# Optimization experiments

Measured on AMD Instinct MI355X. Metric: run time of the kernel, lower is better.

## Reference

```python
import math
import jax, jax.numpy as jnp
import numpy as np

DIM = 512
STYLE_DIM = 512
WS = 8
RES = 64
HEADS = 16
SHIFT = WS // 2
B = 8
EPS = 1e-5


def _rel_pos_index(ws):
    # Faithful replica of the (non-standard) index construction in the source.
    coords = np.stack(np.meshgrid(np.arange(ws), np.arange(ws), indexing='ij')).reshape(2, -1)
    rc = (coords[:, :, None] - coords[:, None, :]).transpose(1, 2, 0).astype(np.int64)
    rc[:, :, 0] += ws - 1
    rc[:, :, 1] += ws - 1
    rc[:, :, 0] += 2 * ws - 1
    return jnp.asarray(rc.sum(-1))  # (ws*ws, ws*ws)


def _attn_mask2(res, ws):
    shift = ws // 2
    m = np.zeros((res, res), dtype=np.float32)
    cnt = 0
    for hs in [slice(0, -ws), slice(-ws, -shift), slice(-shift, None)]:
        for wsl in [slice(0, -ws), slice(-ws, -shift), slice(-shift, None)]:
            m[hs, wsl] = cnt
            cnt += 1
    mw = m.reshape(res // ws, ws, res // ws, ws).transpose(0, 2, 1, 3).reshape(-1, ws * ws)
    am = mw[:, None, :] - mw[:, :, None]  # (nW, N, N)
    return jnp.asarray(np.where(am != 0, -100.0, 0.0).astype(np.float32))


_RPI = _rel_pos_index(WS)
_MASK2 = _attn_mask2(RES, WS)


def _win_part(x, ws):
    Bc, H, W, C = x.shape
    x = x.reshape(Bc, H // ws, ws, W // ws, ws, C).transpose(0, 1, 3, 2, 4, 5)
    return x.reshape(-1, ws * ws, C)


def _win_rev(x, ws, H, W):
    nH, nW = H // ws, W // ws
    C = x.shape[-1]
    x = x.reshape(-1, nH, nW, ws, ws, C).transpose(0, 1, 3, 2, 4, 5)
    return x.reshape(-1, H, W, C)


def _adain(x, style, w, b):
    # x: (B, N, C); InstanceNorm1d over the token dim N per channel (biased var, no affine).
    scale = 1.0 / math.sqrt(w.shape[1])
    s = style @ (w * scale).T + b  # (B, 2C)
    C = x.shape[-1]
    gamma, beta = s[:, :C], s[:, C:]
    mean = x.mean(axis=1, keepdims=True)
    var = x.var(axis=1, keepdims=True)
    xn = (x - mean) / jnp.sqrt(var + EPS)
    return gamma[:, None, :] * xn + beta[:, None, :]


def _window_attn(q, k, v, ws, heads, rpb, rpi, mask):
    # q/k/v: (B, H, W, C)
    C = q.shape[-1]
    hd = C // heads
    qk_scale = hd ** -0.5
    qw = _win_part(q, ws)  # (Bw, N, C)
    kw = _win_part(k, ws)
    vw = _win_part(v, ws)
    Bw, N, _ = qw.shape
    qw = qw.reshape(Bw, N, heads, hd).transpose(0, 2, 1, 3)
    kw = kw.reshape(Bw, N, heads, hd).transpose(0, 2, 1, 3)
    vw = vw.reshape(Bw, N, heads, hd).transpose(0, 2, 1, 3)
    attn = jnp.einsum('bhnd,bhmd->bhnm', qw, kw) * qk_scale
    bias = rpb[rpi.reshape(-1)].reshape(N, N, heads).transpose(2, 0, 1)  # (h, N, N)
    attn = attn + bias[None]
    if mask is not None:
        nW = mask.shape[0]
        attn = attn.reshape(Bw // nW, nW, heads, N, N) + mask[None, :, None]
        attn = attn.reshape(Bw, heads, N, N)
    attn = jax.nn.softmax(attn, axis=-1)
    out = jnp.einsum('bhnm,bhmd->bhnd', attn, vw)
    return out.transpose(0, 2, 1, 3).reshape(Bw, N, C)


def _forward(x, style, ada1_w, ada1_b, qkv_w, qkv_b, rpb1, rpb2,
             proj_w, proj_b, ada2_w, ada2_b, mlp_w1, mlp_b1, mlp_w2, mlp_b2):
    H = W = RES
    Bc, N, C = x.shape
    shortcut = x
    xn = _adain(x, style, ada1_w, ada1_b)
    qkv = xn @ qkv_w.T + qkv_b  # (B, N, 3C)
    qkv = qkv.reshape(Bc, N, 3, C).transpose(2, 0, 1, 3).reshape(3, Bc, H, W, C)
    qkv1 = qkv[..., : C // 2]
    qkv2 = qkv[..., C // 2:]
    qkv2 = jnp.roll(qkv2, shift=(-SHIFT, -SHIFT), axis=(2, 3))
    x1 = _window_attn(qkv1[0], qkv1[1], qkv1[2], WS, HEADS // 2, rpb1, _RPI, None)
    x2 = _window_attn(qkv2[0], qkv2[1], qkv2[2], WS, HEADS // 2, rpb2, _RPI, _MASK2)
    x1 = _win_rev(x1, WS, H, W)
    x2 = _win_rev(x2, WS, H, W)
    x2 = jnp.roll(x2, shift=(SHIFT, SHIFT), axis=(1, 2))
    out = jnp.concatenate([x1, x2], axis=-1).reshape(Bc, N, C)
    out = out @ proj_w.T + proj_b
    out = shortcut + out
    xn2 = _adain(out, style, ada2_w, ada2_b)
    h = xn2 @ mlp_w1.T + mlp_b1
    h = jax.nn.gelu(h, approximate=False)  # erf-based gelu matches source
    h = h @ mlp_w2.T + mlp_b2
    return out + h


def setup_inputs() -> dict:
    key = jax.random.key(0)
    ks = jax.random.split(key, 16)
    rn = lambda k, shp, s: jax.random.normal(k, shp, dtype=jnp.float32) * s
    return {
        'x': rn(ks[0], (B, RES * RES, DIM), 1.0),
        'style': rn(ks[1], (B, STYLE_DIM), 1.0),
        'ada1_w': rn(ks[2], (2 * DIM, STYLE_DIM), 1.0),
        'ada1_b': rn(ks[3], (2 * DIM,), 0.02),
        'qkv_w': rn(ks[4], (3 * DIM, DIM), 0.02),
        'qkv_b': rn(ks[5], (3 * DIM,), 0.02),
        'rpb1': rn(ks[6], ((2 * WS - 1) ** 2, HEADS // 2), 0.02),
        'rpb2': rn(ks[7], ((2 * WS - 1) ** 2, HEADS // 2), 0.02),
        'proj_w': rn(ks[8], (DIM, DIM), 0.02),
        'proj_b': rn(ks[9], (DIM,), 0.02),
        'ada2_w': rn(ks[10], (2 * DIM, STYLE_DIM), 1.0),
        'ada2_b': rn(ks[11], (2 * DIM,), 0.02),
        'mlp_w1': rn(ks[12], (4 * DIM, DIM), 0.02),
        'mlp_b1': rn(ks[13], (4 * DIM,), 0.02),
        'mlp_w2': rn(ks[14], (DIM, 4 * DIM), 0.02),
        'mlp_b2': rn(ks[15], (DIM,), 0.02),
    }


def reference(x, style, ada1_w, ada1_b, qkv_w, qkv_b, rpb1, rpb2,
              proj_w, proj_b, ada2_w, ada2_b, mlp_w1, mlp_b1, mlp_w2, mlp_b2):
    return _forward(x, style, ada1_w, ada1_b, qkv_w, qkv_b, rpb1, rpb2,
                    proj_w, proj_b, ada2_w, ada2_b, mlp_w1, mlp_b1, mlp_w2, mlp_b2)
```

## Files before the change

### kernel.cpp

```cpp
#include <hip/hip_runtime.h>
#include <math.h>

typedef __attribute__((ext_vector_type(8))) short short8;
typedef __attribute__((ext_vector_type(4))) float f32x4;
typedef unsigned short ushort_t;
typedef unsigned long long ull_t;

__device__ __forceinline__ float bf2f(ushort_t u) {
    return __uint_as_float(((unsigned int)u) << 16);
}
__device__ __forceinline__ ushort_t f2bf(float f) {
    unsigned int u = __float_as_uint(f);
    unsigned int r = u + 0x7fffu + ((u >> 16) & 1u);
    return (ushort_t)(r >> 16);
}
__device__ __forceinline__ unsigned cvt_pk_bf16(float lo, float hi) {
    unsigned r;
    asm volatile("v_cvt_pk_bf16_f32 %0, %1, %2" : "=v"(r) : "v"(lo), "v"(hi));
    return r;
}

__device__ __forceinline__ void async_cp16(const void* g, void* l) {
    __builtin_amdgcn_global_load_lds((const __attribute__((address_space(1))) void*)g,
                                     (__attribute__((address_space(3))) void*)l, 16, 0, 0);
}

__device__ __forceinline__ float fast_gelu(float v) {
    float u2 = 2.0f * v * (0.7978845608028654f + 0.0356774081f * v * v);
    float e = __expf(u2);
    float r = 1.0f / (e + 1.0f);
    return v - v * r;
}

__global__ __launch_bounds__(256) void conv_zero(
        const float* __restrict__ qkv_w, ushort_t* __restrict__ qkv_wb,
        const float* __restrict__ proj_w, ushort_t* __restrict__ proj_wb,
        const float* __restrict__ w1, ushort_t* __restrict__ w1b,
        const float* __restrict__ w2, ushort_t* __restrict__ w2b,
        float* __restrict__ psum2, float* __restrict__ psq2,
        const float* __restrict__ rpb1, const float* __restrict__ rpb2,
        float* __restrict__ tbl0, float* __restrict__ tbl1) {
    int i = blockIdx.x * 256 + threadIdx.x;
    if (i < 786432) {
        qkv_wb[i] = f2bf(qkv_w[i]);
    } else if (i < 1048576) {
        int j = i - 786432; proj_wb[j] = f2bf(proj_w[j]);
    } else if (i < 2097152) {
        int j = i - 1048576; w1b[j] = f2bf(w1[j]);
    } else if (i < 3145728) {
        int j = i - 2097152; w2b[j] = f2bf(w2[j]);
    } else if (i < 3153920) {
        int j = i - 3145728;
        psum2[j] = 0.f; psq2[j] = 0.f;
    } else {
        int t = i - 3153920;
        if (t < 32768) {
            int h = t >> 12, ij = t & 4095;
            int qi = ij >> 6, kj = ij & 63;
            int idx = ((qi >> 3) - (kj >> 3)) + ((qi & 7) - (kj & 7)) + 29;
            tbl0[t] = rpb1[idx * 8 + h];
        } else {
            int u = t - 32768;
            int ij = u & 4095;
            int cls = (u >> 12) & 3;
            int h = u >> 14;
            int qi = ij >> 6, kj = ij & 63;
            int idx = ((qi >> 3) - (kj >> 3)) + ((qi & 7) - (kj & 7)) + 29;
            float v = rpb2[idx * 8 + h];
            int gh_i = (cls & 2) ? (((qi >> 3) < 4) ? 1 : 2) : 0;
            int gw_i = (cls & 1) ? (((qi & 7) < 4) ? 1 : 2) : 0;
            int gh_j = (cls & 2) ? (((kj >> 3) < 4) ? 1 : 2) : 0;
            int gw_j = (cls & 1) ? (((kj & 7) < 4) ? 1 : 2) : 0;
            if (gh_i * 3 + gw_i != gh_j * 3 + gw_j) v -= 100.f;
            tbl1[u] = v;
        }
    }
}

__global__ __launch_bounds__(256) void style_kernel(const float* __restrict__ style,
        const float* __restrict__ w1, const float* __restrict__ b1,
        const float* __restrict__ w2, const float* __restrict__ b2,
        float* __restrict__ s1, float* __restrict__ s2) {
    int t = blockIdx.x * 256 + threadIdx.x;
    int which = t >> 13;
    int idx = t & 8191;
    int b = idx >> 10, j = idx & 1023;
    const float* w = which ? w2 : w1;
    const float* bb = which ? b2 : b1;
    const float* st = style + b * 512;
    const float* wr = w + (size_t)j * 512;
    float acc = 0.f;
    for (int k = 0; k < 512; ++k) acc += st[k] * wr[k];
    float v = acc * 0.04419417382415922f + bb[j];
    (which ? s2 : s1)[idx] = v;
}

__global__ __launch_bounds__(512) void stats_part(const float* __restrict__ x,
        float* __restrict__ psum, float* __restrict__ psq) {
    int b = blockIdx.x >> 5;
    int ch = blockIdx.x & 31;
    int c = threadIdx.x;
    const float* p = x + ((size_t)b * 4096 + (size_t)ch * 128) * 512 + c;
    float s = 0.f, q = 0.f;
    for (int t = 0; t < 128; ++t) {
        float v = p[(size_t)t * 512];
        s += v; q += v * v;
    }
    psum[(size_t)blockIdx.x * 512 + c] = s;
    psq [(size_t)blockIdx.x * 512 + c] = q;
}

__global__ __launch_bounds__(256) void stats_fin(const float* __restrict__ psum,
        const float* __restrict__ psq, float* __restrict__ mean, float* __restrict__ rstd) {
    int i = blockIdx.x * 256 + threadIdx.x;
    int b = i >> 9, c = i & 511;
    float s = 0.f, q = 0.f;
    for (int ch = 0; ch < 32; ++ch) {
        s += psum[(size_t)(b * 32 + ch) * 512 + c];
        q += psq [(size_t)(b * 32 + ch) * 512 + c];
    }
    float m = s * (1.f / 4096.f);
    float v = q * (1.f / 4096.f) - m * m;
    mean[i] = m;
    rstd[i] = rsqrtf(v + 1e-5f);
}

__global__ __launch_bounds__(256) void stats_fin2(const float* __restrict__ psum2,
        const float* __restrict__ psq2, float* __restrict__ mean, float* __restrict__ rstd) {
    int i = blockIdx.x * 256 + threadIdx.x;
    float m = psum2[i] * (1.f / 4096.f);
    float v = psq2[i] * (1.f / 4096.f) - m * m;
    mean[i] = m;
    rstd[i] = rsqrtf(v + 1e-5f);
}

__global__ __launch_bounds__(256) void adain_kernel(const float* __restrict__ x,
        const float* __restrict__ s, const float* __restrict__ mean,
        const float* __restrict__ rstd, ushort_t* __restrict__ xn) {
    size_t i4 = (size_t)blockIdx.x * 256 + threadIdx.x;
    size_t e = i4 * 4;
    int b = (int)(e >> 21);
    int c = (int)(e & 511);
    float4 xv = *(const float4*)(x + e);
    float vals[4] = {xv.x, xv.y, xv.z, xv.w};
    ushort_t o[4];
#pragma unroll
    for (int j = 0; j < 4; ++j) {
        int cc = c + j;
        float g  = s[b * 1024 + cc];
        float be = s[b * 1024 + 512 + cc];
        float mn = mean[b * 512 + cc];
        float rs = rstd[b * 512 + cc];
        o[j] = f2bf(g * (vals[j] - mn) * rs + be);
    }
    ull_t packed = (ull_t)o[0] |
        ((ull_t)o[1] << 16) | ((ull_t)o[2] << 32) | ((ull_t)o[3] << 48);
    *(ull_t*)(xn + e) = packed;
}

template<int EPI>
__global__ __launch_bounds__(512, 2) void gemm256(
        const ushort_t* __restrict__ A, const ushort_t* __restrict__ Bw,
        const float* __restrict__ bias, const float* __restrict__ resid,
        float* __restrict__ outf, ushort_t* __restrict__ outh,
        float* __restrict__ psum2, float* __restrict__ psq2,
        int N, int K, int gridN, int ntiles, int lnt) {
    __shared__ ushort_t lds[65536];
    const int tid  = threadIdx.x;
    const int lane = tid & 63;
    const int wave = tid >> 6;
    const int wm = wave >> 2, wn = wave & 3;
    const int lm = lane & 15;
    const int kg = lane >> 4;
    const int nt = 1 << lnt;
    const int tpb = ntiles >> 8;

    const int orig = blockIdx.x;
    const int wgid = (orig & 7) * 32 + (orig >> 3);

    unsigned int lo0 = lm * 128 + ((kg * 16) ^ ((lm & 7) << 4));
    unsigned int lo1 = lo0 ^ 64;
    unsigned int vA0 = wm * 16384 + lo0;
    unsigned int vA1 = wm * 16384 + lo1;
    unsigned int vB0 = 65536 + (wn >> 1) * 16384 + (wn & 1) * 8192 + lo0;
    unsigned int vB1 = 65536 + (wn >> 1) * 16384 + (wn & 1) * 8192 + lo1;
    const char* ldsc = (const char*)lds;

    int off[2][2];
#pragma unroll
    for (int rnd = 0; rnd < 2; ++rnd) {
        int chunk = tid + rnd * 512;
        int row = chunk >> 3;
        int g = chunk & 7;
        int gsw = g ^ (row & 7);
#pragma unroll
        for (int h = 0; h < 2; ++h)
            off[h][rnd] = (h * 128 + row) * K + gsw * 8;
    }

    f32x4 acc[8][4];
#pragma unroll
    for (int m = 0; m < 8; ++m)
#pragma unroll
        for (int n = 0; n < 4; ++n)
#pragma unroll
            for (int r = 0; r < 4; ++r) acc[m][n][r] = 0.f;

    auto stage = [&](const ushort_t* __restrict__ mat, long bcur, long bnxt,
                     int dslot, int h, int tt, int isB) {
        long mb = (tt < nt) ? bcur : bnxt;
        int kt = tt & (nt - 1);
        const ushort_t* base = mat + mb + (kt << 6);
        ushort_t* dst = (ushort_t*)lds + isB * 32768 + dslot * 16384 + h * 8192 + tid * 8;
#pragma unroll
        for (int rnd = 0; rnd < 2; ++rnd)
            async_cp16(base + off[h][rnd], dst + rnd * 4096);
    };

    int tcur = wgid;
    int bm = tcur / gridN, bn = tcur - bm * gridN;
    long Am = (long)bm * 256 * K;
    long Bn = (long)bn * 256 * K;

    stage(A,  Am, Am, 0, 0, 0, 0); stage(A,  Am, Am, 0, 1, 0, 0);
    stage(Bw, Bn, Bn, 0, 0, 0, 1); stage(Bw, Bn, Bn, 0, 1, 0, 1);
    stage(Bw, Bn, Bn, 1, 0, 1, 1); stage(Bw, Bn, Bn, 1, 1, 1, 1);
    asm volatile("s_waitcnt vmcnt(4)" ::: "memory");
    __builtin_amdgcn_sched_barrier(0);
    __builtin_amdgcn_s_barrier();

    for (int ti = 0; ti < tpb; ++ti) {
        int tnxt = (ti + 1 < tpb) ? tcur + 256 : tcur;
        int bm2 = tnxt / gridN, bn2 = tnxt - bm2 * gridN;
        long Am2 = (long)bm2 * 256 * K;
        long Bn2 = (long)bn2 * 256 * K;

#pragma unroll 2
        for (int t = 0; t < nt; ++t) {
            const int c = t & 1;
            short8 bfr[4][2];
#pragma unroll
            for (int q = 0; q < 4; ++q) {
                short8 af[2][2];
#pragma unroll
                for (int mq = 0; mq < 2; ++mq) {
                    af[mq][0] = *(const short8*)(ldsc + vA0 + (q * 4096 + mq * 2048));
                    af[mq][1] = *(const short8*)(ldsc + vA1 + (q * 4096 + mq * 2048));
                }
                if (q == 0) {
#pragma unroll
                    for (int n = 0; n < 4; ++n) {
                        bfr[n][0] = *(const short8*)(ldsc + vB0 + n * 2048);
                        bfr[n][1] = *(const short8*)(ldsc + vB1 + n * 2048);
                    }
                }
                if      (q == 0) stage(A,  Am, Am2, c ^ 1, 0, t + 1, 0);
                else if (q == 1) stage(A,  Am, Am2, c ^ 1, 1, t + 1, 0);
                else if (q == 2) stage(Bw, Bn, Bn2, c,     0, t + 2, 1);
                else             stage(Bw, Bn, Bn2, c,     1, t + 2, 1);

                __builtin_amdgcn_s_barrier();
                asm volatile("s_waitcnt lgkmcnt(0)" ::: "memory");
                __builtin_amdgcn_sched_barrier(0);
                __builtin_amdgcn_s_setprio(1);
#pragma unroll
                for (int mq = 0; mq < 2; ++mq)
#pragma unroll
                    for (int n = 0; n < 4; ++n)
#pragma unroll
                        for (int ks = 0; ks < 2; ++ks)
                            acc[q * 2 + mq][n] = __builtin_amdgcn_mfma_f32_16x16x32_bf16(
                                af[mq][ks], bfr[n][ks], acc[q * 2 + mq][n], 0, 0, 0);
                __builtin_amdgcn_s_setprio(0);
                if (q == 3) {
                    asm volatile("s_waitcnt vmcnt(4)" ::: "memory");
                    __builtin_amdgcn_sched_barrier(0);
                }
                __builtin_amdgcn_s_barrier();
            }
            vA0 ^= 32768u; vA1 ^= 32768u; vB0 ^= 32768u; vB1 ^= 32768u;
        }

        const long tile_m = (long)bm * 256;
        const long tile_n = (long)bn * 256;
        float csum[4], csq[4];
        if (EPI == 1) {
#pragma unroll
            for (int n = 0; n < 4; ++n) { csum[n] = 0.f; csq[n] = 0.f; }
        }
#pragma unroll
        for (int m = 0; m < 8; ++m) {
            long row0 = tile_m + wm * 128 + m * 16 + kg * 4;
#pragma unroll
            for (int n = 0; n < 4; ++n) {
                long col = tile_n + wn * 64 + n * 16 + lm;
                float bb = bias[col];
#pragma unroll
                for (int r = 0; r < 4; ++r) {
                    long o = (row0 + r) * (long)N + col;
                    float v = acc[m][n][r] + bb;
                    if (EPI == 0) {
                        outh[o] = f2bf(v);
                    } else if (EPI == 1) {
                        float w = v + resid[o];
                        outf[o] = w;
                        csum[n] += w; csq[n] += w * w;
                    } else if (EPI == 2) {
                        outh[o] = f2bf(fast_gelu(v));
                    } else {
                        outf[o] += v;
                    }
                    acc[m][n][r] = 0.f;
                }
            }
        }
        if (EPI == 1) {
            int b = (int)(tile_m >> 12);
#pragma unroll
            for (int n = 0; n < 4; ++n) {
                int col = (int)(tile_n + wn * 64 + n * 16 + lm);
                atomicAdd(&psum2[b * 512 + col], csum[n]);
                atomicAdd(&psq2 [b * 512 + col], csq[n]);
            }
        }

        tcur = tnxt; bm = bm2; bn = bn2; Am = Am2; Bn = Bn2;
    }
}

__global__ __launch_bounds__(256) void attn_mfma(const ushort_t* __restrict__ qkv,
        const float* __restrict__ tbl0, const float* __restrict__ tbl1,
        ushort_t* __restrict__ attno) {
    __shared__ ushort_t lds[27648];
    const int tid = threadIdx.x;
    const int lane = tid & 63;
    const int wave = tid >> 6;
    const int job = blockIdx.x * 4 + wave;
    const int branch = job >> 12;
    const int w_idx  = (job >> 3) & 511;
    const int head   = job & 7;
    const int b = w_idx >> 6, win = w_idx & 63;
    const int wh = win >> 3, ww = win & 7;
    const int c0 = branch * 256 + head * 32;
    const int i_lo = lane & 15;
    const int kg = lane >> 4;

    ushort_t* Vt = lds + wave * 6912;
    ushort_t* P  = lds + wave * 6912 + 2304;

    auto tokof = [&](int p) {
        int hh = wh * 8 + (p >> 3), wp = ww * 8 + (p & 7);
        if (branch) { hh = (hh + 4) & 63; wp = (wp + 4) & 63; }
        return b * 4096 + hh * 64 + wp;
    };

    {
        const ushort_t* vp = qkv + (size_t)tokof(lane) * 1536 + 1024 + c0;
        short8 v0 = *(const short8*)(vp);
        short8 v1 = *(const short8*)(vp + 8);
        short8 v2 = *(const short8*)(vp + 16);
        short8 v3 = *(const short8*)(vp + 24);
#pragma unroll
        for (int e = 0; e < 8; ++e) {
            Vt[(e     ) * 72 + lane] = (ushort_t)v0[e];
            Vt[(e +  8) * 72 + lane] = (ushort_t)v1[e];
            Vt[(e + 16) * 72 + lane] = (ushort_t)v2[e];
            Vt[(e + 24) * 72 + lane] = (ushort_t)v3[e];
        }
    }

    short8 kf[4], qf[4];
#pragma unroll
    for (int m = 0; m < 4; ++m) {
        size_t rowb = (size_t)tokof(m * 16 + i_lo) * 1536;
        kf[m] = *(const short8*)(qkv + rowb + 512 + c0 + kg * 8);
        qf[m] = *(const short8*)(qkv + rowb + c0 + kg * 8);
    }

    f32x4 s[4][4];
#pragma unroll
    for (int mj = 0; mj < 4; ++mj)
#pragma unroll
        for (int ni = 0; ni < 4; ++ni)
#pragma unroll
            for (int r = 0; r < 4; ++r) s[mj][ni][r] = 0.f;
#pragma unroll
    for (int mj = 0; mj < 4; ++mj)
#pragma unroll
        for (int ni = 0; ni < 4; ++ni)
            s[mj][ni] = __builtin_amdgcn_mfma_f32_16x16x32_bf16(kf[mj], qf[ni], s[mj][ni], 0, 0, 0);

    const float* tb;
    if (branch == 0) {
        tb = tbl0 + head * 4096;
    } else {
        int cls = ((wh == 7) ? 2 : 0) | ((ww == 7) ? 1 : 0);
        tb = tbl1 + (head * 4 + cls) * 4096;
    }
#pragma unroll
    for (int ni = 0; ni < 4; ++ni) {
        int i = ni * 16 + i_lo;
#pragma unroll
        for (int mj = 0; mj < 4; ++mj) {
            float4 bv = *(const float4*)(tb + i * 64 + mj * 16 + kg * 4);
            s[mj][ni][0] = s[mj][ni][0] * 0.17677669529663687f + bv.x;
            s[mj][ni][1] = s[mj][ni][1] * 0.17677669529663687f + bv.y;
            s[mj][ni][2] = s[mj][ni][2] * 0.17677669529663687f + bv.z;
            s[mj][ni][3] = s[mj][ni][3] * 0.17677669529663687f + bv.w;
        }
    }

    float mx[4], rs[4];
#pragma unroll
    for (int ni = 0; ni < 4; ++ni) {
        float m = -1e30f;
#pragma unroll
        for (int mj = 0; mj < 4; ++mj)
#pragma unroll
            for (int r = 0; r < 4; ++r) m = fmaxf(m, s[mj][ni][r]);
        m = fmaxf(m, __shfl_xor(m, 16));
        m = fmaxf(m, __shfl_xor(m, 32));
        mx[ni] = m;
    }
#pragma unroll
    for (int ni = 0; ni < 4; ++ni) {
        float sum = 0.f;
#pragma unroll
        for (int mj = 0; mj < 4; ++mj)
#pragma unroll
            for (int r = 0; r < 4; ++r) {
                float e = __expf(s[mj][ni][r] - mx[ni]);
                s[mj][ni][r] = e;
                sum += e;
            }
        sum += __shfl_xor(sum, 16);
        sum += __shfl_xor(sum, 32);
        rs[ni] = sum;
    }

#pragma unroll
    for (int ni = 0; ni < 4; ++ni) {
        int i = ni * 16 + i_lo;
#pragma unroll
        for (int mj = 0; mj < 4; ++mj) {
            unsigned w0 = cvt_pk_bf16(s[mj][ni][0], s[mj][ni][1]);
            unsigned w1 = cvt_pk_bf16(s[mj][ni][2], s[mj][ni][3]);
            ull_t w = (ull_t)w0 | ((ull_t)w1 << 32);
            *(ull_t*)&P[i * 72 + mj * 16 + kg * 4] = w;
        }
    }
    asm volatile("s_waitcnt lgkmcnt(0)" ::: "memory");
    __builtin_amdgcn_sched_barrier(0);

    short8 va[2][2];
    short8 pb[4][2];
#pragma unroll
    for (int md = 0; md < 2; ++md)
#pragma unroll
        for (int ks = 0; ks < 2; ++ks)
            va[md][ks] = *(const short8*)&Vt[(md * 16 + i_lo) * 72 + ks * 32 + kg * 8];
#pragma unroll
    for (int ni = 0; ni < 4; ++ni)
#pragma unroll
        for (int ks = 0; ks < 2; ++ks)
            pb[ni][ks] = *(const short8*)&P[(ni * 16 + i_lo) * 72 + ks * 32 + kg * 8];

    f32x4 o[2][4];
#pragma unroll
    for (int md = 0; md < 2; ++md)
#pragma unroll
        for (int ni = 0; ni < 4; ++ni)
#pragma unroll
            for (int r = 0; r < 4; ++r) o[md][ni][r] = 0.f;
#pragma unroll
    for (int md = 0; md < 2; ++md)
#pragma unroll
        for (int ni = 0; ni < 4; ++ni)
#pragma unroll
            for (int ks = 0; ks < 2; ++ks)
                o[md][ni] = __builtin_amdgcn_mfma_f32_16x16x32_bf16(va[md][ks], pb[ni][ks], o[md][ni], 0, 0, 0);

#pragma unroll
    for (int ni = 0; ni < 4; ++ni) {
        float inv = 1.f / rs[ni];
        ushort_t* op = attno + (size_t)tokof(ni * 16 + i_lo) * 512 + c0;
#pragma unroll
        for (int md = 0; md < 2; ++md) {
            ushort_t h0 = f2bf(o[md][ni][0] * inv);
            ushort_t h1 = f2bf(o[md][ni][1] * inv);
            ushort_t h2 = f2bf(o[md][ni][2] * inv);
            ushort_t h3 = f2bf(o[md][ni][3] * inv);
            ull_t w = (ull_t)h0 | ((ull_t)h1 << 16) | ((ull_t)h2 << 32) | ((ull_t)h3 << 48);
            *(ull_t*)(op + md * 16 + kg * 4) = w;
        }
    }
}

extern "C" void kernel_launch(void* const* d_in, const int* in_sizes, int n_in,
                              void* d_out, int out_size, void* d_ws, size_t ws_size,
                              hipStream_t stream) {
    const float* x      = (const float*)d_in[0];
    const float* style  = (const float*)d_in[1];
    const float* ada1_w = (const float*)d_in[2];
    const float* ada1_b = (const float*)d_in[3];
    const float* qkv_w  = (const float*)d_in[4];
    const float* qkv_b  = (const float*)d_in[5];
    const float* rpb1   = (const float*)d_in[6];
    const float* rpb2   = (const float*)d_in[7];
    const float* proj_w = (const float*)d_in[8];
    const float* proj_b = (const float*)d_in[9];
    const float* ada2_w = (const float*)d_in[10];
    const float* ada2_b = (const float*)d_in[11];
    const float* mlp_w1 = (const float*)d_in[12];
    const float* mlp_b1 = (const float*)d_in[13];
    const float* mlp_w2 = (const float*)d_in[14];
    const float* mlp_b2 = (const float*)d_in[15];
    float* outf = (float*)d_out;

    char* W = (char*)d_ws;
    ushort_t* qkvb    = (ushort_t*)(W);
    ushort_t* attno   = (ushort_t*)(W + 100663296);
    ushort_t* hbuf    = (ushort_t*)(W);
    ushort_t* xn      = (ushort_t*)(W + 134217728);
    ushort_t* qkv_wb  = (ushort_t*)(W + 167772160);
    ushort_t* proj_wb = (ushort_t*)(W + 167772160 + 1572864);
    ushort_t* w1b     = (ushort_t*)(W + 167772160 + 2097152);
    ushort_t* w2b     = (ushort_t*)(W + 167772160 + 4194304);
    float* freg  = (float*)(W + 167772160 + 6291456);
    float* s1    = freg;
    float* s2    = freg + 8192;
    float* mean1 = freg + 16384;
    float* rstd1 = freg + 20480;
    float* mean2 = freg + 24576;
    float* rstd2 = freg + 28672;
    float* psum  = freg + 32768;
    float* psq   = freg + 163840;
    float* psum2 = freg + 294912;
    float* psq2  = freg + 303104;
    float* tbl0  = freg + 311296;
    float* tbl1  = freg + 344064;

    conv_zero<<<12960, 256, 0, stream>>>(qkv_w, qkv_wb, proj_w, proj_wb,
                                         mlp_w1, w1b, mlp_w2, w2b, psum2, psq2,
                                         rpb1, rpb2, tbl0, tbl1);

    style_kernel<<<64, 256, 0, stream>>>(style, ada1_w, ada1_b, ada2_w, ada2_b, s1, s2);

    stats_part<<<256, 512, 0, stream>>>(x, psum, psq);
    stats_fin<<<16, 256, 0, stream>>>(psum, psq, mean1, rstd1);
    adain_kernel<<<16384, 256, 0, stream>>>(x, s1, mean1, rstd1, xn);

    gemm256<0><<<256, 512, 0, stream>>>(xn, qkv_wb, qkv_b, nullptr, nullptr, qkvb,
                                        nullptr, nullptr, 1536, 512, 6, 768, 3);

    attn_mfma<<<2048, 256, 0, stream>>>(qkvb, tbl0, tbl1, attno);

    gemm256<1><<<256, 512, 0, stream>>>(attno, proj_wb, proj_b, x, outf, nullptr,
                                        psum2, psq2, 512, 512, 2, 256, 3);

    stats_fin2<<<16, 256, 0, stream>>>(psum2, psq2, mean2, rstd2);
    adain_kernel<<<16384, 256, 0, stream>>>(outf, s2, mean2, rstd2, xn);

    gemm256<2><<<256, 512, 0, stream>>>(xn, w1b, mlp_b1, nullptr, nullptr, hbuf,
                                        nullptr, nullptr, 2048, 512, 8, 1024, 3);
    gemm256<3><<<256, 512, 0, stream>>>(hbuf, w2b, mlp_b2, nullptr, outf, nullptr,
                                        nullptr, nullptr, 512, 2048, 2, 256, 5);
}
```

Before: 443.1 us.

## Load B fragments directly from global into registers, halve LDS in GEMM

The GEMM no longer stages the weight (B) tile through LDS. Each wave loads its B MFMA fragments straight from global memory into double-buffered registers, one k-tile ahead, while A keeps its async LDS double buffer. This halves LDS use and drops the B LDS reads and async copies, aiming for higher occupancy and less LDS traffic. In exchange the B reads are uncoalesced, each wave fetches B data that other waves also need, and the wait becomes vmcnt(0), so global latency may be exposed.

```diff
diff --git a/kernel.cpp b/kernel.cpp
--- a/kernel.cpp
+++ b/kernel.cpp
@@ -165,7 +165,7 @@
         float* __restrict__ outf, ushort_t* __restrict__ outh,
         float* __restrict__ psum2, float* __restrict__ psq2,
         int N, int K, int gridN, int ntiles, int lnt) {
-    __shared__ ushort_t lds[65536];
+    __shared__ ushort_t lds[32768];
     const int tid  = threadIdx.x;
     const int lane = tid & 63;
     const int wave = tid >> 6;
@@ -179,14 +179,11 @@
     const int wgid = (orig & 7) * 32 + (orig >> 3);
 
     unsigned int lo0 = lm * 128 + ((kg * 16) ^ ((lm & 7) << 4));
-    unsigned int lo1 = lo0 ^ 64;
     unsigned int vA0 = wm * 16384 + lo0;
-    unsigned int vA1 = wm * 16384 + lo1;
-    unsigned int vB0 = 65536 + (wn >> 1) * 16384 + (wn & 1) * 8192 + lo0;
-    unsigned int vB1 = 65536 + (wn >> 1) * 16384 + (wn & 1) * 8192 + lo1;
+    unsigned int vA1 = vA0 ^ 64;
     const char* ldsc = (const char*)lds;
 
-    int off[2][2];
+    int offA[2][2];
 #pragma unroll
     for (int rnd = 0; rnd < 2; ++rnd) {
         int chunk = tid + rnd * 512;
@@ -195,8 +192,13 @@
         int gsw = g ^ (row & 7);
 #pragma unroll
         for (int h = 0; h < 2; ++h)
-            off[h][rnd] = (h * 128 + row) * K + gsw * 8;
-    }
+            offA[h][rnd] = (h * 128 + row) * K + gsw * 8;
+    }
+
+    long rowB[4];
+#pragma unroll
+    for (int n = 0; n < 4; ++n)
+        rowB[n] = (long)(wn * 64 + n * 16 + lm) * K + kg * 8;
 
     f32x4 acc[8][4];
 #pragma unroll
@@ -206,79 +208,91 @@
 #pragma unroll
             for (int r = 0; r < 4; ++r) acc[m][n][r] = 0.f;
 
-    auto stage = [&](const ushort_t* __restrict__ mat, long bcur, long bnxt,
-                     int dslot, int h, int tt, int isB) {
+    auto stageA = [&](long bcur, long bnxt, int dslot, int tt) {
         long mb = (tt < nt) ? bcur : bnxt;
         int kt = tt & (nt - 1);
-        const ushort_t* base = mat + mb + (kt << 6);
-        ushort_t* dst = (ushort_t*)lds + isB * 32768 + dslot * 16384 + h * 8192 + tid * 8;
-#pragma unroll
-        for (int rnd = 0; rnd < 2; ++rnd)
-            async_cp16(base + off[h][rnd], dst + rnd * 4096);
+        const ushort_t* base = A + mb + (kt << 6);
+        ushort_t* dst = (ushort_t*)lds + dslot * 16384 + tid * 8;
+        async_cp16(base + offA[0][0], dst);
+        async_cp16(base + offA[0][1], dst + 4096);
+        async_cp16(base + offA[1][0], dst + 8192);
+        async_cp16(base + offA[1][1], dst + 12288);
     };
+
+    short8 bX[4][2], bY[4][2];
 
     int tcur = wgid;
     int bm = tcur / gridN, bn = tcur - bm * gridN;
     long Am = (long)bm * 256 * K;
     long Bn = (long)bn * 256 * K;
-
-    stage(A,  Am, Am, 0, 0, 0, 0); stage(A,  Am, Am, 0, 1, 0, 0);
-    stage(Bw, Bn, Bn, 0, 0, 0, 1); stage(Bw, Bn, Bn, 0, 1, 0, 1);
-    stage(Bw, Bn, Bn, 1, 0, 1, 1); stage(Bw, Bn, Bn, 1, 1, 1, 1);
-    asm volatile("s_waitcnt vmcnt(4)" ::: "memory");
+    long Am2 = Am, Bn2 = Bn;
+
+    stageA(Am, Am, 0, 0);
+    {
+        const ushort_t* bp = Bw + Bn;
+#pragma unroll
+        for (int n = 0; n < 4; ++n) {
+            bX[n][0] = *(const short8*)(bp + rowB[n]);
+            bX[n][1] = *(const short8*)(bp + rowB[n] + 32);
+        }
+    }
+    asm volatile("s_waitcnt vmcnt(0)" ::: "memory");
     __builtin_amdgcn_sched_barrier(0);
     __builtin_amdgcn_s_barrier();
+
+    auto ktile = [&](int t, short8 (&bnow)[4][2], short8 (&bnext)[4][2]) {
+        const int c = t & 1;
+        const int tt1 = t + 1;
+        const long Bb = (tt1 < nt) ? Bn : Bn2;
+        const int kt1 = tt1 & (nt - 1);
+#pragma unroll
+        for (int q = 0; q < 4; ++q) {
+            short8 af[2][2];
+#pragma unroll
+            for (int mq = 0; mq < 2; ++mq) {
+                af[mq][0] = *(const short8*)(ldsc + vA0 + (q * 4096 + mq * 2048));
+                af[mq][1] = *(const short8*)(ldsc + vA1 + (q * 4096 + mq * 2048));
+            }
+            if (q == 0) stageA(Am, Am2, c ^ 1, tt1);
+            if (q == 1) {
+                const ushort_t* bp = Bw + Bb + (kt1 << 6);
+#pragma unroll
+                for (int n = 0; n < 4; ++n) {
+                    bnext[n][0] = *(const short8*)(bp + rowB[n]);
+                    bnext[n][1] = *(const short8*)(bp + rowB[n] + 32);
+                }
+            }
+            __builtin_amdgcn_s_barrier();
+            asm volatile("s_waitcnt lgkmcnt(0)" ::: "memory");
+            __builtin_amdgcn_sched_barrier(0);
+            __builtin_amdgcn_s_setprio(1);
+#pragma unroll
+            for (int mq = 0; mq < 2; ++mq)
+#pragma unroll
+                for (int n = 0; n < 4; ++n)
+#pragma unroll
+                    for (int ks = 0; ks < 2; ++ks)
+                        acc[q * 2 + mq][n] = __builtin_amdgcn_mfma_f32_16x16x32_bf16(
+                            af[mq][ks], bnow[n][ks], acc[q * 2 + mq][n], 0, 0, 0);
+            __builtin_amdgcn_s_setprio(0);
+            if (q == 3) {
+                asm volatile("s_waitcnt vmcnt(0)" ::: "memory");
+                __builtin_amdgcn_sched_barrier(0);
+            }
+            __builtin_amdgcn_s_barrier();
+        }
+        vA0 ^= 32768u; vA1 ^= 32768u;
+    };
 
     for (int ti = 0; ti < tpb; ++ti) {
         int tnxt = (ti + 1 < tpb) ? tcur + 256 : tcur;
         int bm2 = tnxt / gridN, bn2 = tnxt - bm2 * gridN;
-        long Am2 = (long)bm2 * 256 * K;
-        long Bn2 = (long)bn2 * 256 * K;
-
-#pragma unroll 2
-        for (int t = 0; t < nt; ++t) {
-            const int c = t & 1;
-            short8 bfr[4][2];
-#pragma unroll
-            for (int q = 0; q < 4; ++q) {
-                short8 af[2][2];
-#pragma unroll
-                for (int mq = 0; mq < 2; ++mq) {
-                    af[mq][0] = *(const short8*)(ldsc + vA0 + (q * 4096 + mq * 2048));
-                    af[mq][1] = *(const short8*)(ldsc + vA1 + (q * 4096 + mq * 2048));
-                }
-                if (q == 0) {
-#pragma unroll
-                    for (int n = 0; n < 4; ++n) {
-                        bfr[n][0] = *(const short8*)(ldsc + vB0 + n * 2048);
-                        bfr[n][1] = *(const short8*)(ldsc + vB1 + n * 2048);
-                    }
-                }
-                if      (q == 0) stage(A,  Am, Am2, c ^ 1, 0, t + 1, 0);
-                else if (q == 1) stage(A,  Am, Am2, c ^ 1, 1, t + 1, 0);
-                else if (q == 2) stage(Bw, Bn, Bn2, c,     0, t + 2, 1);
-                else             stage(Bw, Bn, Bn2, c,     1, t + 2, 1);
-
-                __builtin_amdgcn_s_barrier();
-                asm volatile("s_waitcnt lgkmcnt(0)" ::: "memory");
-                __builtin_amdgcn_sched_barrier(0);
-                __builtin_amdgcn_s_setprio(1);
-#pragma unroll
-                for (int mq = 0; mq < 2; ++mq)
-#pragma unroll
-                    for (int n = 0; n < 4; ++n)
-#pragma unroll
-                        for (int ks = 0; ks < 2; ++ks)
-                            acc[q * 2 + mq][n] = __builtin_amdgcn_mfma_f32_16x16x32_bf16(
-                                af[mq][ks], bfr[n][ks], acc[q * 2 + mq][n], 0, 0, 0);
-                __builtin_amdgcn_s_setprio(0);
-                if (q == 3) {
-                    asm volatile("s_waitcnt vmcnt(4)" ::: "memory");
-                    __builtin_amdgcn_sched_barrier(0);
-                }
-                __builtin_amdgcn_s_barrier();
-            }
-            vA0 ^= 32768u; vA1 ^= 32768u; vB0 ^= 32768u; vB1 ^= 32768u;
+        Am2 = (long)bm2 * 256 * K;
+        Bn2 = (long)bn2 * 256 * K;
+
+        for (int t2 = 0; t2 < nt; t2 += 2) {
+            ktile(t2, bX, bY);
+            ktile(t2 + 1, bY, bX);
         }
 
         const long tile_m = (long)bm * 256;
```

New measurement: 577.3 us. +30.3%, slower.

## Stage bf16 GEMM epilogue through LDS for vector stores and drop an inner barrier

Applied to the files above, without the earlier changes.

For the bf16-output epilogues (plain bias and GELU), each wave now converts its accumulators to packed bf16, writes them into a per-wave LDS slab, and reads them back as rows. It can then issue 16-byte coalesced global stores in place of scattered 2-byte stores. Separately, the per-quarter s_barrier plus lgkmcnt wait before the MFMA block in the main K loop is removed, leaving a single barrier per step. The LDS slab reuses part of the pipelined A/B staging buffers, and there is now less synchronisation in the inner loop. Both could race with in-flight async copies for the next tile if the ordering is not otherwise guaranteed.

```diff
diff --git a/kernel.cpp b/kernel.cpp
--- a/kernel.cpp
+++ b/kernel.cpp
@@ -228,6 +228,7 @@
     asm volatile("s_waitcnt vmcnt(4)" ::: "memory");
     __builtin_amdgcn_sched_barrier(0);
     __builtin_amdgcn_s_barrier();
+    asm volatile("" ::: "memory");
 
     for (int ti = 0; ti < tpb; ++ti) {
         int tnxt = (ti + 1 < tpb) ? tcur + 256 : tcur;
@@ -259,9 +260,6 @@
                 else if (q == 2) stage(Bw, Bn, Bn2, c,     0, t + 2, 1);
                 else             stage(Bw, Bn, Bn2, c,     1, t + 2, 1);
 
-                __builtin_amdgcn_s_barrier();
-                asm volatile("s_waitcnt lgkmcnt(0)" ::: "memory");
-                __builtin_amdgcn_sched_barrier(0);
                 __builtin_amdgcn_s_setprio(1);
 #pragma unroll
                 for (int mq = 0; mq < 2; ++mq)
@@ -277,50 +275,89 @@
                     __builtin_amdgcn_sched_barrier(0);
                 }
                 __builtin_amdgcn_s_barrier();
+                asm volatile("" ::: "memory");
             }
             vA0 ^= 32768u; vA1 ^= 32768u; vB0 ^= 32768u; vB1 ^= 32768u;
         }
 
         const long tile_m = (long)bm * 256;
         const long tile_n = (long)bn * 256;
-        float csum[4], csq[4];
-        if (EPI == 1) {
-#pragma unroll
-            for (int n = 0; n < 4; ++n) { csum[n] = 0.f; csq[n] = 0.f; }
-        }
-#pragma unroll
-        for (int m = 0; m < 8; ++m) {
-            long row0 = tile_m + wm * 128 + m * 16 + kg * 4;
-#pragma unroll
-            for (int n = 0; n < 4; ++n) {
-                long col = tile_n + wn * 64 + n * 16 + lm;
-                float bb = bias[col];
-#pragma unroll
-                for (int r = 0; r < 4; ++r) {
-                    long o = (row0 + r) * (long)N + col;
-                    float v = acc[m][n][r] + bb;
-                    if (EPI == 0) {
-                        outh[o] = f2bf(v);
-                    } else if (EPI == 1) {
-                        float w = v + resid[o];
-                        outf[o] = w;
-                        csum[n] += w; csq[n] += w * w;
-                    } else if (EPI == 2) {
-                        outh[o] = f2bf(fast_gelu(v));
-                    } else {
-                        outf[o] += v;
+
+        if (EPI == 0 || EPI == 2) {
+            ushort_t* slab = (ushort_t*)lds + 16384 + wave * 1024;
+            ushort_t* wb = slab + kg * 4 * 64 + lm;
+            const int l8 = lane & 7, lr = lane >> 3;
+            const long growb = tile_m + wm * 128 + lr;
+            const long gcol  = tile_n + wn * 64 + l8 * 8;
+            float bb[4];
+#pragma unroll
+            for (int n = 0; n < 4; ++n) bb[n] = bias[tile_n + wn * 64 + n * 16 + lm];
+#pragma unroll
+            for (int m = 0; m < 8; ++m) {
+#pragma unroll
+                for (int n = 0; n < 4; ++n) {
+                    float v0 = acc[m][n][0] + bb[n];
+                    float v1 = acc[m][n][1] + bb[n];
+                    float v2 = acc[m][n][2] + bb[n];
+                    float v3 = acc[m][n][3] + bb[n];
+                    if (EPI == 2) {
+                        v0 = fast_gelu(v0); v1 = fast_gelu(v1);
+                        v2 = fast_gelu(v2); v3 = fast_gelu(v3);
                     }
-                    acc[m][n][r] = 0.f;
+                    unsigned p01 = cvt_pk_bf16(v0, v1);
+                    unsigned p23 = cvt_pk_bf16(v2, v3);
+                    wb[n * 16 +   0] = (ushort_t)(p01 & 0xffffu);
+                    wb[n * 16 +  64] = (ushort_t)(p01 >> 16);
+                    wb[n * 16 + 128] = (ushort_t)(p23 & 0xffffu);
+                    wb[n * 16 + 192] = (ushort_t)(p23 >> 16);
+                    acc[m][n][0] = 0.f; acc[m][n][1] = 0.f;
+                    acc[m][n][2] = 0.f; acc[m][n][3] = 0.f;
+                }
+                asm volatile("s_waitcnt lgkmcnt(0)" ::: "memory");
+                __builtin_amdgcn_sched_barrier(0);
+                short8 rlo = *(const short8*)(slab + lr * 64 + l8 * 8);
+                short8 rhi = *(const short8*)(slab + (8 + lr) * 64 + l8 * 8);
+                *(short8*)(outh + (growb + m * 16) * (long)N + gcol) = rlo;
+                *(short8*)(outh + (growb + m * 16 + 8) * (long)N + gcol) = rhi;
+            }
+            __builtin_amdgcn_s_barrier();
+            asm volatile("" ::: "memory");
+        } else {
+            float csum[4], csq[4];
+            if (EPI == 1) {
+#pragma unroll
+                for (int n = 0; n < 4; ++n) { csum[n] = 0.f; csq[n] = 0.f; }
+            }
+#pragma unroll
+            for (int m = 0; m < 8; ++m) {
+                long row0 = tile_m + wm * 128 + m * 16 + kg * 4;
+#pragma unroll
+                for (int n = 0; n < 4; ++n) {
+                    long col = tile_n + wn * 64 + n * 16 + lm;
+                    float bb = bias[col];
+#pragma unroll
+                    for (int r = 0; r < 4; ++r) {
+                        long o = (row0 + r) * (long)N + col;
+                        float v = acc[m][n][r] + bb;
+                        if (EPI == 1) {
+                            float w = v + resid[o];
+                            outf[o] = w;
+                            csum[n] += w; csq[n] += w * w;
+                        } else {
+                            outf[o] += v;
+                        }
+                        acc[m][n][r] = 0.f;
+                    }
                 }
             }
-        }
-        if (EPI == 1) {
-            int b = (int)(tile_m >> 12);
-#pragma unroll
-            for (int n = 0; n < 4; ++n) {
-                int col = (int)(tile_n + wn * 64 + n * 16 + lm);
-                atomicAdd(&psum2[b * 512 + col], csum[n]);
-                atomicAdd(&psq2 [b * 512 + col], csq[n]);
+            if (EPI == 1) {
+                int b = (int)(tile_m >> 12);
+#pragma unroll
+                for (int n = 0; n < 4; ++n) {
+                    int col = (int)(tile_n + wn * 64 + n * 16 + lm);
+                    atomicAdd(&psum2[b * 512 + col], csum[n]);
+                    atomicAdd(&psq2 [b * 512 + col], csq[n]);
+                }
             }
         }
 
```

New measurement: 425.7 us. 1.04x faster.
